# Kernel tuning notes

Hardware: AMD Instinct MI355X
Metric: run time of the kernel (lower is better)

The kernel has to match this reference:

```python
import jax, jax.numpy as jnp
import numpy as np

N, D, H, DH, E = 50000, 128, 4, 32, 600000
EPS = 1e-5


def _seg_softmax(logits, seg, n):
    # numerically stable softmax over edges grouped by destination node
    m = jax.ops.segment_max(logits, seg, num_segments=n)
    e = jnp.exp(logits - m[seg])
    s = jax.ops.segment_sum(e, seg, num_segments=n)
    return e / s[seg]


def _bn(x, g, b):
    # BatchNorm1d, training-mode statistics (biased variance), eps=1e-5
    mu = jnp.mean(x, 0)
    var = jnp.mean((x - mu) ** 2, 0)
    return g * (x - mu) * jax.lax.rsqrt(var + EPS) + b


def _gat(x, src, dst, W, a_s, a_d, bias):
    # PyG GATConv: shared lin, additive attention, leaky_relu(0.2), dst-softmax, concat heads + bias
    n = x.shape[0]
    xp = (x @ W).reshape(n, H, DH)
    al_s = jnp.sum(xp * a_s, -1)  # [N,H]
    al_d = jnp.sum(xp * a_d, -1)
    lg = jax.nn.leaky_relu(al_s[src] + al_d[dst], 0.2)  # [E',H]
    alpha = _seg_softmax(lg, dst, n)
    out = jax.ops.segment_sum(alpha[..., None] * xp[src], dst, num_segments=n)
    return out.reshape(n, H * DH) + bias


def setup_inputs() -> dict:
    key = jax.random.key(0)
    ks = jax.random.split(key, 24)
    s = 0.05
    inp = {
        'x_cell': jax.random.normal(ks[0], (N, D), jnp.float32),
        'z_h': jax.random.normal(ks[1], (D,), jnp.float32),
        'x_cell_embedded': jax.random.normal(ks[2], (N, D), jnp.float32),
        'edge_index_0': jax.random.randint(ks[3], (2, E), 0, N, dtype=jnp.int32),
        'edge_index_1': jax.random.randint(ks[4], (2, E), 0, N, dtype=jnp.int32),
        # GAT params, stacked over (conv layer 0/1, edge type 0/1)
        'gat_W': jax.random.normal(ks[5], (2, 2, D, D), jnp.float32) * s,
        'gat_att_src': jax.random.normal(ks[6], (2, 2, H, DH), jnp.float32) * s,
        'gat_att_dst': jax.random.normal(ks[7], (2, 2, H, DH), jnp.float32) * s,
        'gat_bias': jnp.zeros((2, 2, D), jnp.float32),
        # BatchNorm params for bn1, bn2, bn_hgt
        'bn_gamma': jnp.ones((3, D), jnp.float32),
        'bn_beta': jnp.zeros((3, D), jnp.float32),
        # HGTConv params
        'hgt_Wk': jax.random.normal(ks[8], (D, D), jnp.float32) * s,
        'hgt_bk': jnp.zeros((D,), jnp.float32),
        'hgt_Wq': jax.random.normal(ks[9], (D, D), jnp.float32) * s,
        'hgt_bq': jnp.zeros((D,), jnp.float32),
        'hgt_Wv': jax.random.normal(ks[10], (D, D), jnp.float32) * s,
        'hgt_bv': jnp.zeros((D,), jnp.float32),
        'hgt_a_rel': jax.random.normal(ks[11], (2, H, DH, DH), jnp.float32) * s,
        'hgt_m_rel': jax.random.normal(ks[12], (2, H, DH, DH), jnp.float32) * s,
        'hgt_p_rel': jnp.ones((2, H), jnp.float32),
        'hgt_Wo': jax.random.normal(ks[13], (D, D), jnp.float32) * s,
        'hgt_bo': jnp.zeros((D,), jnp.float32),
        'hgt_skip': jnp.float32(1.0),
        # input injection + FiLM
        'inj_W': jax.random.normal(ks[14], (D, D), jnp.float32) * s,
        'inj_b': jnp.zeros((D,), jnp.float32),
        'film_W1': jax.random.normal(ks[15], (D, 2 * D), jnp.float32) * s,
        'film_b1': jnp.zeros((2 * D,), jnp.float32),
        'film_W2': jax.random.normal(ks[16], (2 * D, 2 * D), jnp.float32) * s,
        'film_b2': jnp.zeros((2 * D,), jnp.float32),
    }
    return inp


def reference(x_cell, z_h, x_cell_embedded, edge_index_0, edge_index_1,
              gat_W, gat_att_src, gat_att_dst, gat_bias, bn_gamma, bn_beta,
              hgt_Wk, hgt_bk, hgt_Wq, hgt_bq, hgt_Wv, hgt_bv,
              hgt_a_rel, hgt_m_rel, hgt_p_rel, hgt_Wo, hgt_bo, hgt_skip,
              inj_W, inj_b, film_W1, film_b1, film_W2, film_b2):
    n = x_cell.shape[0]
    loops = jnp.arange(n, dtype=edge_index_0.dtype)
    # GATConv add_self_loops=True: augment each relation's edge list with self loops
    eis = [(jnp.concatenate([ei[0], loops]), jnp.concatenate([ei[1], loops]))
           for ei in (edge_index_0, edge_index_1)]

    def hetero_gat(x, c):
        out = jnp.zeros((n, D), x.dtype)
        for t, (src, dst) in enumerate(eis):  # HeteroConv aggr='sum'
            out = out + _gat(x, src, dst, gat_W[c, t], gat_att_src[c, t], gat_att_dst[c, t], gat_bias[c, t])
        return out

    lrelu = lambda v: jax.nn.leaky_relu(v, 0.2)
    x1 = lrelu(x_cell + _bn(hetero_gat(x_cell, 0), bn_gamma[0], bn_beta[0]))
    x2 = lrelu(x1 + _bn(hetero_gat(x1, 1), bn_gamma[1], bn_beta[1]))

    # HGTConv (single node type, 2 edge types, no self loops)
    k = (x2 @ hgt_Wk + hgt_bk).reshape(n, H, DH)
    q = (x2 @ hgt_Wq + hgt_bq).reshape(n, H, DH)
    v = (x2 @ hgt_Wv + hgt_bv).reshape(n, H, DH)
    lgs, msgs, dsts = [], [], []
    inv_sqrt = np.float32(1.0 / np.sqrt(DH))
    for t, ei in enumerate((edge_index_0, edge_index_1)):
        src, dst = ei[0], ei[1]
        kt = jnp.einsum('nhd,hde->nhe', k, hgt_a_rel[t])  # relation-transformed keys
        vt = jnp.einsum('nhd,hde->nhe', v, hgt_m_rel[t])  # relation-transformed values
        lgs.append(jnp.sum(q[dst] * kt[src], -1) * hgt_p_rel[t] * inv_sqrt)  # [E,H]
        msgs.append(vt[src])
        dsts.append(dst)
    lg = jnp.concatenate(lgs)
    msg = jnp.concatenate(msgs)
    dst_all = jnp.concatenate(dsts)
    alpha = _seg_softmax(lg, dst_all, n)  # softmax over all incoming edges (all relations)
    agg = jax.ops.segment_sum(alpha[..., None] * msg, dst_all, num_segments=n).reshape(n, H * DH)
    hgt_out = jax.nn.gelu(agg, approximate=False) @ hgt_Wo + hgt_bo
    sk = jax.nn.sigmoid(hgt_skip)
    x3 = sk * hgt_out + (1.0 - sk) * x2

    x3 = _bn(x3, bn_gamma[2], bn_beta[2])
    x3 = lrelu(x2 + x3)
    x3 = x3 + x_cell_embedded @ inj_W + inj_b

    # FiLM on global z_h
    hzh = jax.nn.gelu(z_h @ film_W1 + film_b1, approximate=False)
    gb = hzh @ film_W2 + film_b2
    gamma, beta = gb[:D], gb[D:]
    return gamma * x3 + beta
```

## Files before the change

kernel.cpp:

```cpp
#include <hip/hip_runtime.h>
#include <math.h>

#define NN 50000
#define DD 128
#define HH 4
#define DHH 32
#define EE 600000
#define N2 (2*NN)
#define NBLK 256

typedef unsigned short u16;
typedef unsigned int   u32;
using short8 = __attribute__((ext_vector_type(8))) short;
using f32x4  = __attribute__((ext_vector_type(4))) float;

#define LOG2E 1.44269504f

__device__ __forceinline__ float lrelu(float v){ return v > 0.f ? v : 0.2f*v; }
__device__ __forceinline__ float gelu_exact(float x){ return 0.5f*x*(1.f+erff(x*0.70710678118654752f)); }
__device__ __forceinline__ u16 f2bf(float f){
  u32 u = __float_as_uint(f);
  u32 r = (u + 0x7fffu + ((u>>16)&1u)) >> 16;
  return (u16)r;
}
__device__ __forceinline__ u32 pack2bf(float a, float b){ return (u32)f2bf(a) | ((u32)f2bf(b)<<16); }
__device__ __forceinline__ float bflo(u32 u){ return __uint_as_float(u<<16); }
__device__ __forceinline__ float bfhi(u32 u){ return __uint_as_float(u & 0xffff0000u); }

__global__ __launch_bounds__(256) void prep_all(
    const float* __restrict__ gat_W, const float* __restrict__ Wk, const float* __restrict__ Wv,
    const float* __restrict__ Wo, const float* __restrict__ injW, u16* __restrict__ WT,
    const float* __restrict__ Wq, const float* __restrict__ bq, const float* __restrict__ a_rel,
    u16* __restrict__ wqtT, float* __restrict__ bqt,
    const float* __restrict__ z, const float* __restrict__ fW1, const float* __restrict__ fb1,
    const float* __restrict__ fW2, const float* __restrict__ fb2, float* __restrict__ gb){
  __shared__ float t[32][33];
  __shared__ float hsh[256];
  const int bid = blockIdx.x;
  if(bid < 128){
    const int m = bid >> 4, tile = bid & 15, tr = tile>>2, tc = tile&3;
    const float* src = (m<4) ? (gat_W + (size_t)m*16384) : (m==4? Wk : m==5? Wv : m==6? Wo : injW);
    const int lr = threadIdx.x>>5, lc = threadIdx.x&31;
    #pragma unroll
    for(int p=0;p<4;++p) t[lr+p*8][lc] = src[(size_t)(tr*32+lr+p*8)*128 + tc*32+lc];
    __syncthreads();
    #pragma unroll
    for(int p=0;p<4;++p)
      WT[(size_t)m*16384 + (size_t)(tc*32+lr+p*8)*128 + tr*32+lc] = f2bf(t[lc][lr+p*8]);
  } else if(bid < 257){
    int idx = (bid-128)*256 + threadIdx.x;
    if(idx < 2*128*129){
      int tt = idx / (128*129);
      int r = idx % (128*129);
      int f = r / 129, c = r % 129;
      int h = f>>5, m = f&31;
      const float* srcp = (c<128) ? (Wq + (size_t)c*128 + h*DHH) : (bq + h*DHH);
      const float* arow = a_rel + (((size_t)(tt*HH+h)*DHH)+m)*DHH;
      float s=0.f;
      #pragma unroll
      for(int e=0;e<DHH;++e) s = fmaf(srcp[e], arow[e], s);
      if(c<128) wqtT[(size_t)tt*16384 + (size_t)f*128 + c] = f2bf(s);
      else      bqt[tt*128 + f] = s;
    }
  } else {
    int j = threadIdx.x;
    float acc = fb1[j];
    for(int d=0; d<DD; ++d) acc = fmaf(z[d], fW1[d*256+j], acc);
    hsh[j] = gelu_exact(acc);
    __syncthreads();
    float acc2 = fb2[j];
    for(int k=0;k<256;++k) acc2 = fmaf(hsh[k], fW2[k*256+j], acc2);
    gb[j] = acc2;
  }
}

__global__ void count2_kernel(const int* __restrict__ d0, const int* __restrict__ d1, int* __restrict__ jcnt){
  int e = blockIdx.x*blockDim.x+threadIdx.x;
  if(e < EE)        atomicAdd(&jcnt[d0[e]], 1);
  else if(e < 2*EE) atomicAdd(&jcnt[NN + d1[e-EE]], 1);
}

__global__ void scan_partial(const int* __restrict__ cnt, int* __restrict__ bsum){
  int t = threadIdx.x;
  int i0 = blockIdx.x*512 + 2*t;
  int s = 0;
  if(i0   < N2) s += cnt[i0];
  if(i0+1 < N2) s += cnt[i0+1];
  __shared__ int red[256];
  red[t]=s; __syncthreads();
  for(int off=128; off>0; off>>=1){ if(t<off) red[t]+=red[t+off]; __syncthreads(); }
  if(t==0) bsum[blockIdx.x]=red[0];
}

__global__ void scan_final2(const int* __restrict__ cnt, const int* __restrict__ bsum,
                            int* __restrict__ jrs, int* __restrict__ jcur, int nb){
  __shared__ int sh[256];
  int t = threadIdx.x;
  {
    int v = (t<nb)? bsum[t] : 0;
    sh[t]=v; __syncthreads();
    for(int off=1; off<256; off<<=1){
      int u = (t>=off)? sh[t-off] : 0; __syncthreads();
      sh[t]+=u; __syncthreads();
    }
  }
  const int bofsv = sh[blockIdx.x] - bsum[blockIdx.x];
  if(blockIdx.x==0 && t==0) jrs[N2] = sh[nb-1];
  __syncthreads();
  int i0 = blockIdx.x*512 + 2*t;
  int a = (i0   < N2)? cnt[i0]   : 0;
  int c = (i0+1 < N2)? cnt[i0+1] : 0;
  int s = a+c;
  sh[t]=s; __syncthreads();
  for(int off=1; off<256; off<<=1){
    int u = (t>=off)? sh[t-off] : 0; __syncthreads();
    sh[t]+=u; __syncthreads();
  }
  int ex = bofsv + sh[t]-s;
  if(i0   < N2){ jrs[i0]=ex;     jcur[i0]=ex; }
  if(i0+1 < N2){ jrs[i0+1]=ex+a; jcur[i0+1]=ex+a; }
}

__global__ void fill2_kernel(const int* __restrict__ ei0, const int* __restrict__ ei1,
                             int* __restrict__ jcur, u16* __restrict__ es){
  int e = blockIdx.x*blockDim.x+threadIdx.x;
  if(e < EE){
    int d = ei0[EE+e];
    int pos = atomicAdd(&jcur[d],1);
    es[pos] = (u16)ei0[e];
  } else if(e < 2*EE){
    int i = e-EE;
    int d = ei1[EE+i];
    int pos = atomicAdd(&jcur[NN+d],1);
    es[pos] = (u16)ei1[i];
  }
}

constexpr int MM_BIAS  = 1;
constexpr int MM_FILM  = 2;
constexpr int MM_SKIP  = 4;
constexpr int MM_ATT   = 8;
constexpr int MM_ABF16 = 64;

#define SWZ(row, byte) ((byte) ^ (((row)&7)<<4))

template<int MODE>
__device__ __forceinline__ void mgemm_core(const void* Av, const u16* WT, int row0, int n,
                                           u16* Al, u16* Wl, f32x4 (&acc)[8]){
  const int tid = threadIdx.x;
  if(MODE & MM_ABF16){
    const uint2* Ag = (const uint2*)((const u16*)Av + (size_t)row0*128);
    const int maxv = (min(64, n-row0))*32;
    #pragma unroll
    for(int j=0;j<8;++j){
      int v = tid + j*256;
      uint2 st = make_uint2(0u,0u);
      if(v < maxv) st = Ag[v];
      int row = v>>5, cb = (v&31)*8;
      *(uint2*)((char*)Al + row*256 + SWZ(row, cb)) = st;
    }
  } else {
    const float4* Ag = (const float4*)((const float*)Av + (size_t)row0*128);
    const int maxv = (min(64, n-row0))*32;
    #pragma unroll
    for(int j=0;j<8;++j){
      int v = tid + j*256;
      float4 val = make_float4(0.f,0.f,0.f,0.f);
      if(v < maxv) val = Ag[v];
      int row = v>>5, cb = (v&31)*8;
      uint2 st; st.x = pack2bf(val.x, val.y); st.y = pack2bf(val.z, val.w);
      *(uint2*)((char*)Al + row*256 + SWZ(row, cb)) = st;
    }
  }
  {
    const u32* Wg = (const u32*)WT;
    #pragma unroll
    for(int j=0;j<32;++j){
      int v = tid + j*256;
      u32 w = Wg[v];
      int row = v>>6, cb = (v&63)*4;
      *(u32*)((char*)Wl + row*256 + SWZ(row, cb)) = w;
    }
  }
  __syncthreads();
  const int lane = tid & 63;
  const int wv   = tid >> 6;
  const int r16  = lane & 15;
  const int kg   = lane >> 4;
  #pragma unroll
  for(int nn=0;nn<8;++nn) acc[nn] = (f32x4){0.f,0.f,0.f,0.f};
  #pragma unroll
  for(int s=0;s<4;++s){
    const int arow = wv*16 + r16;
    const int kb = s*64 + kg*16;
    short8 af = *(const short8*)((const char*)Al + arow*256 + SWZ(arow, kb));
    #pragma unroll
    for(int nn=0;nn<8;++nn){
      const int brow = nn*16 + r16;
      short8 bf = *(const short8*)((const char*)Wl + brow*256 + SWZ(brow, kb));
      acc[nn] = __builtin_amdgcn_mfma_f32_16x16x32_bf16(af, bf, acc[nn], 0, 0, 0);
    }
  }
}

template<int MODE>
__global__ __launch_bounds__(256) void mgemm(const void* __restrict__ Av, const u16* __restrict__ WT,
    const float* __restrict__ bias, const float* __restrict__ base, const float* __restrict__ fgb,
    const float* __restrict__ skipv, float* __restrict__ C, int n){
  __shared__ u16 Al[64*128];
  __shared__ u16 Wl[128*128];
  const int row0 = blockIdx.x*64;
  f32x4 acc[8];
  mgemm_core<MODE>(Av, WT, row0, n, Al, Wl, acc);
  const int lane = threadIdx.x & 63;
  const int wv   = threadIdx.x >> 6;
  const int r16  = lane & 15;
  const int kg   = lane >> 4;
  float bvals[8];
  if(MODE & MM_BIAS){
    #pragma unroll
    for(int nn=0;nn<8;++nn) bvals[nn] = bias[nn*16+r16];
  }
  float sk = 0.f;
  if(MODE & MM_SKIP) sk = 1.f/(1.f+__expf(-skipv[0]));
  #pragma unroll
  for(int i=0;i<4;++i){
    const int row = row0 + wv*16 + kg*4 + i;
    if(row >= n) continue;
    #pragma unroll
    for(int nn=0;nn<8;++nn){
      const int col = nn*16 + r16;
      float o = acc[nn][i];
      if(MODE & MM_BIAS) o += bvals[nn];
      if(MODE & MM_SKIP)
        o = sk*o + (1.f-sk)*base[(size_t)row*128 + col];
      if(MODE & MM_FILM){
        o += base[(size_t)row*128 + col];
        o = fgb[col]*o + fgb[128+col];
      }
      C[(size_t)row*128 + col] = o;
    }
  }
}

struct MJob {
  const u16* WT;
  const float* bias;
  const float* as_;
  const float* ad_;
  void* Cv;
  int att_t;
  int sel;
};
struct MJobs { MJob j[4]; };

template<int MODE>
__global__ __launch_bounds__(256) void mgemmJ(const float* __restrict__ Av, MJobs jobs,
    float* __restrict__ als8, float* __restrict__ ald8, int blocksPerJob, int n){
  __shared__ u16 Al[64*128];
  __shared__ u16 Wl[128*128];
  const MJob job = jobs.j[blockIdx.x / blocksPerJob];
  const int row0 = (blockIdx.x % blocksPerJob)*64;
  f32x4 acc[8];
  mgemm_core<MODE>(Av, job.WT, row0, n, Al, Wl, acc);
  const int lane = threadIdx.x & 63;
  const int wv   = threadIdx.x >> 6;
  const int r16  = lane & 15;
  const int kg   = lane >> 4;
  if(MODE & MM_ATT){
    float asv[8], adv[8];
    #pragma unroll
    for(int nn=0;nn<8;++nn){ asv[nn]=job.as_[nn*16+r16]; adv[nn]=job.ad_[nn*16+r16]; }
    #pragma unroll
    for(int i=0;i<4;++i){
      const int row = row0 + wv*16 + kg*4 + i;
      #pragma unroll
      for(int h=0;h<4;++h){
        float ps = asv[2*h]*acc[2*h][i] + asv[2*h+1]*acc[2*h+1][i];
        float pd = adv[2*h]*acc[2*h][i] + adv[2*h+1]*acc[2*h+1][i];
        ps += __shfl_xor(ps,1); ps += __shfl_xor(ps,2); ps += __shfl_xor(ps,4); ps += __shfl_xor(ps,8);
        pd += __shfl_xor(pd,1); pd += __shfl_xor(pd,2); pd += __shfl_xor(pd,4); pd += __shfl_xor(pd,8);
        if(row < n && r16 == 0){
          als8[(size_t)row*8 + 2*h + job.att_t] = ps;
          ald8[(size_t)row*8 + 2*h + job.att_t] = pd;
        }
      }
    }
  }
  float bvals[8];
  if(MODE & MM_BIAS){
    #pragma unroll
    for(int nn=0;nn<8;++nn) bvals[nn] = job.bias[nn*16+r16];
  }
  #pragma unroll
  for(int i=0;i<4;++i){
    const int row = row0 + wv*16 + kg*4 + i;
    if(row >= n) continue;
    #pragma unroll
    for(int nn=0;nn<8;++nn){
      const int col = nn*16 + r16;
      float o = acc[nn][i];
      if(MODE & MM_BIAS) o += bvals[nn];
      if(job.sel == 1)
        ((u16*)job.Cv)[(size_t)row*128 + col] = f2bf(o);
      else
        *(u16*)((char*)job.Cv + (size_t)row*512 + (col>>1)*8 + (col&1)*2 + (job.sel-2)*4) = f2bf(o);
    }
  }
}

__global__ __launch_bounds__(256) void gat_gather3(const u16* __restrict__ xp0, const u16* __restrict__ xp1,
    const float* __restrict__ als8, const float* __restrict__ ald8,
    const int* __restrict__ jrs, const u16* __restrict__ es,
    const float* __restrict__ gb0, const float* __restrict__ gb1, float* __restrict__ out){
  const int gid = blockIdx.x*blockDim.x + threadIdx.x;
  const int node = gid >> 6;
  const int lane = threadIdx.x & 63;
  if(node >= NN) return;
  const int h = lane >> 4;
  const int cc = 2*lane;
  float o0 = gb0[cc] + gb1[cc], o1 = gb0[cc+1] + gb1[cc+1];
  #pragma unroll
  for(int t=0;t<2;++t){
    const u16* __restrict__ xp = t ? xp1 : xp0;
    const float aldv = ald8[(size_t)node*8 + 2*h + t];
    const int s0 = jrs[t*NN+node], s1 = jrs[t*NN+node+1];
    float ssum=0.f, a0=0.f, a1=0.f;
    int p = s0;
    for(; p+3<s1; p+=4){
      const int sA = es[p], sB = es[p+1], sC = es[p+2], sD = es[p+3];
      const u32 xA = *(const u32*)&xp[(size_t)sA*DD + cc];
      const u32 xB = *(const u32*)&xp[(size_t)sB*DD + cc];
      const u32 xC = *(const u32*)&xp[(size_t)sC*DD + cc];
      const u32 xD = *(const u32*)&xp[(size_t)sD*DD + cc];
      float lA = als8[(size_t)sA*8 + 2*h + t] + aldv;
      float lB = als8[(size_t)sB*8 + 2*h + t] + aldv;
      float lC = als8[(size_t)sC*8 + 2*h + t] + aldv;
      float lD = als8[(size_t)sD*8 + 2*h + t] + aldv;
      const float eA = exp2f(lA>0.f ? lA*LOG2E : lA*(0.2f*LOG2E));
      const float eB = exp2f(lB>0.f ? lB*LOG2E : lB*(0.2f*LOG2E));
      const float eC = exp2f(lC>0.f ? lC*LOG2E : lC*(0.2f*LOG2E));
      const float eD = exp2f(lD>0.f ? lD*LOG2E : lD*(0.2f*LOG2E));
      ssum += (eA+eB)+(eC+eD);
      a0 = fmaf(eA, bflo(xA), a0); a1 = fmaf(eA, bfhi(xA), a1);
      a0 = fmaf(eB, bflo(xB), a0); a1 = fmaf(eB, bfhi(xB), a1);
      a0 = fmaf(eC, bflo(xC), a0); a1 = fmaf(eC, bfhi(xC), a1);
      a0 = fmaf(eD, bflo(xD), a0); a1 = fmaf(eD, bfhi(xD), a1);
    }
    for(; p<s1; ++p){
      const int sA = es[p];
      const u32 xA = *(const u32*)&xp[(size_t)sA*DD + cc];
      float lA = als8[(size_t)sA*8 + 2*h + t] + aldv;
      const float eA = exp2f(lA>0.f ? lA*LOG2E : lA*(0.2f*LOG2E));
      ssum += eA;
      a0 = fmaf(eA, bflo(xA), a0); a1 = fmaf(eA, bfhi(xA), a1);
    }
    {
      float lg = als8[(size_t)node*8 + 2*h + t] + aldv;
      const float ev = exp2f(lg>0.f ? lg*LOG2E : lg*(0.2f*LOG2E));
      ssum += ev;
      const u32 xr = *(const u32*)&xp[(size_t)node*DD + cc];
      a0 = fmaf(ev, bflo(xr), a0); a1 = fmaf(ev, bfhi(xr), a1);
    }
    const float inv = 1.f/ssum;
    o0 = fmaf(a0, inv, o0); o1 = fmaf(a1, inv, o1);
  }
  *(float2*)&out[(size_t)node*DD + cc] = make_float2(o0, o1);
}

__global__ __launch_bounds__(256) void bn_stats_fused(const float* __restrict__ X, float* __restrict__ part,
                               const float* __restrict__ gamma, const float* __restrict__ beta,
                               float* __restrict__ stat, int* __restrict__ counter){
  const int f = threadIdx.x & 127, rg = threadIdx.x>>7;
  float s=0.f, s2=0.f;
  for(int r = blockIdx.x*2+rg; r<NN; r += NBLK*2){
    float v = X[(size_t)r*DD+f]; s+=v; s2 = fmaf(v,v,s2);
  }
  __shared__ float ls[256], ls2[256];
  __shared__ int lastsh;
  ls[threadIdx.x]=s; ls2[threadIdx.x]=s2; __syncthreads();
  if(rg==0){
    part[blockIdx.x*256 + f]       = ls[f]+ls[128+f];
    part[blockIdx.x*256 + 128 + f] = ls2[f]+ls2[128+f];
  }
  __threadfence();
  if(threadIdx.x==0) lastsh = (atomicAdd(counter,1) == NBLK-1);
  __syncthreads();
  if(lastsh){
    __threadfence();
    float ss=0.f, ss2=0.f;
    #pragma unroll 8
    for(int bk=rg; bk<NBLK; bk+=2){
      ss  += part[bk*256 + f];
      ss2 += part[bk*256 + 128 + f];
    }
    __syncthreads();
    ls[threadIdx.x]=ss; ls2[threadIdx.x]=ss2;
    __syncthreads();
    if(rg==0){
      float S1 = ls[f]+ls[128+f], S2 = ls2[f]+ls2[128+f];
      float mu = S1/(float)NN;
      float var = S2/(float)NN - mu*mu;
      float rs = rsqrtf(var+1e-5f);
      stat[f]     = gamma[f]*rs;
      stat[128+f] = beta[f] - gamma[f]*rs*mu;
    }
    if(threadIdx.x==0) *counter = 0;
  }
}

__global__ void bn_apply_lrelu(const float* __restrict__ xprev, const float* __restrict__ acc,
                               const float* __restrict__ stat, float* __restrict__ out){
  int idx = blockIdx.x*blockDim.x+threadIdx.x;
  if(idx >= NN*64) return;
  int c = (2*idx) & 127;
  float2 x = ((const float2*)xprev)[idx];
  float2 a = ((const float2*)acc)[idx];
  float o0 = lrelu(x.x + fmaf(stat[c],   a.x, stat[128+c]));
  float o1 = lrelu(x.y + fmaf(stat[c+1], a.y, stat[128+c+1]));
  ((float2*)out)[idx] = make_float2(o0,o1);
}

__global__ __launch_bounds__(256) void hgt_merged2(const u16* __restrict__ qt,
    const u32* __restrict__ kv, const int* __restrict__ jrs, const u16* __restrict__ es,
    const float* __restrict__ p_rel, u16* __restrict__ Sv){
  const int gid = blockIdx.x*blockDim.x + threadIdx.x;
  const int node = gid >> 6;
  const int lane = threadIdx.x & 63;
  if(node >= NN) return;
  const int h = lane >> 4;
  float acc[2][2] = {{0.f,0.f},{0.f,0.f}};
  float ssum = 0.f;
  #pragma unroll
  for(int t=0;t<2;++t){
    const u32 qw = *(const u32*)&qt[(size_t)t*NN*DD + (size_t)node*DD + 2*lane];
    const float q0 = bflo(qw), q1 = bfhi(qw);
    const float scale2 = p_rel[t*HH+h]*(0.17677669529663687f*LOG2E);
    const int s0 = jrs[t*NN+node], s1 = jrs[t*NN+node+1];
    int p = s0;
    for(; p+3<s1; p+=4){
      const int sA = es[p], sB = es[p+1], sC = es[p+2], sD = es[p+3];
      const uint2 kA = *(const uint2*)&kv[(size_t)sA*128 + 2*lane];
      const uint2 kB = *(const uint2*)&kv[(size_t)sB*128 + 2*lane];
      const uint2 kC = *(const uint2*)&kv[(size_t)sC*128 + 2*lane];
      const uint2 kD = *(const uint2*)&kv[(size_t)sD*128 + 2*lane];
      float pA = q0*bflo(kA.x) + q1*bfhi(kA.x);
      float pB = q0*bflo(kB.x) + q1*bfhi(kB.x);
      float pC = q0*bflo(kC.x) + q1*bfhi(kC.x);
      float pD = q0*bflo(kD.x) + q1*bfhi(kD.x);
      pA += __shfl_xor(pA,1); pB += __shfl_xor(pB,1); pC += __shfl_xor(pC,1); pD += __shfl_xor(pD,1);
      pA += __shfl_xor(pA,2); pB += __shfl_xor(pB,2); pC += __shfl_xor(pC,2); pD += __shfl_xor(pD,2);
      pA += __shfl_xor(pA,4); pB += __shfl_xor(pB,4); pC += __shfl_xor(pC,4); pD += __shfl_xor(pD,4);
      pA += __shfl_xor(pA,8); pB += __shfl_xor(pB,8); pC += __shfl_xor(pC,8); pD += __shfl_xor(pD,8);
      const float eA=exp2f(pA*scale2), eB=exp2f(pB*scale2);
      const float eC=exp2f(pC*scale2), eD=exp2f(pD*scale2);
      ssum += (eA+eB)+(eC+eD);
      acc[t][0] = fmaf(eA, bflo(kA.y), acc[t][0]); acc[t][1] = fmaf(eA, bfhi(kA.y), acc[t][1]);
      acc[t][0] = fmaf(eB, bflo(kB.y), acc[t][0]); acc[t][1] = fmaf(eB, bfhi(kB.y), acc[t][1]);
      acc[t][0] = fmaf(eC, bflo(kC.y), acc[t][0]); acc[t][1] = fmaf(eC, bfhi(kC.y), acc[t][1]);
      acc[t][0] = fmaf(eD, bflo(kD.y), acc[t][0]); acc[t][1] = fmaf(eD, bfhi(kD.y), acc[t][1]);
    }
    for(; p<s1; ++p){
      const int sA = es[p];
      const uint2 kA = *(const uint2*)&kv[(size_t)sA*128 + 2*lane];
      float pA = q0*bflo(kA.x) + q1*bfhi(kA.x);
      pA += __shfl_xor(pA,1); pA += __shfl_xor(pA,2); pA += __shfl_xor(pA,4); pA += __shfl_xor(pA,8);
      const float eA = exp2f(pA*scale2);
      ssum += eA;
      acc[t][0] = fmaf(eA, bflo(kA.y), acc[t][0]); acc[t][1] = fmaf(eA, bfhi(kA.y), acc[t][1]);
    }
  }
  const float inv = ssum>0.f ? 1.f/ssum : 0.f;
  ((u32*)&Sv[(size_t)node*256 +       2*lane])[0] = pack2bf(acc[0][0]*inv, acc[0][1]*inv);
  ((u32*)&Sv[(size_t)node*256 + 128 + 2*lane])[0] = pack2bf(acc[1][0]*inv, acc[1][1]*inv);
}

__global__ __launch_bounds__(256) void mtransform_kernel(const u16* __restrict__ Sv, const float* __restrict__ m_rel,
                                                         u16* __restrict__ out){
  __shared__ float Msh[2*HH*DHH*DHH];
  for(int i=threadIdx.x;i<2*HH*DHH*DHH;i+=256) Msh[i]=m_rel[i];
  __syncthreads();
  int idx = blockIdx.x*blockDim.x + threadIdx.x;
  if(idx >= NN*DD) return;
  int node = idx>>7, f = idx&127, h = f>>5, e = f&31;
  const u16* s0p = &Sv[(size_t)node*256 + h*DHH];
  const u16* s1p = &Sv[(size_t)node*256 + 128 + h*DHH];
  const float* M0 = &Msh[(0*HH+h)*DHH*DHH + e];
  const float* M1 = &Msh[(1*HH+h)*DHH*DHH + e];
  float s = 0.f;
  #pragma unroll
  for(int d=0; d<DHH; d+=2){
    u32 w0 = *(const u32*)&s0p[d];
    u32 w1 = *(const u32*)&s1p[d];
    s = fmaf(bflo(w0), M0[d*DHH],     s);
    s = fmaf(bfhi(w0), M0[(d+1)*DHH], s);
    s = fmaf(bflo(w1), M1[d*DHH],     s);
    s = fmaf(bfhi(w1), M1[(d+1)*DHH], s);
  }
  out[idx] = f2bf(gelu_exact(s));
}

extern "C" void kernel_launch(void* const* d_in, const int* in_sizes, int n_in,
                              void* d_out, int out_size, void* d_ws, size_t ws_size,
                              hipStream_t stream){
  const float* x_cell = (const float*)d_in[0];
  const float* z_h    = (const float*)d_in[1];
  const float* x_emb  = (const float*)d_in[2];
  const int*   ei0    = (const int*)d_in[3];
  const int*   ei1    = (const int*)d_in[4];
  const float* gat_W  = (const float*)d_in[5];
  const float* gat_as = (const float*)d_in[6];
  const float* gat_ad = (const float*)d_in[7];
  const float* gat_b  = (const float*)d_in[8];
  const float* bn_g   = (const float*)d_in[9];
  const float* bn_b   = (const float*)d_in[10];
  const float* Wk = (const float*)d_in[11];
  const float* bk = (const float*)d_in[12];
  const float* Wq = (const float*)d_in[13];
  const float* bq = (const float*)d_in[14];
  const float* Wv = (const float*)d_in[15];
  const float* bv = (const float*)d_in[16];
  const float* a_rel = (const float*)d_in[17];
  const float* m_rel = (const float*)d_in[18];
  const float* p_rel = (const float*)d_in[19];
  const float* Wo = (const float*)d_in[20];
  const float* bo = (const float*)d_in[21];
  const float* skip = (const float*)d_in[22];
  const float* injW = (const float*)d_in[23];
  const float* injb = (const float*)d_in[24];
  const float* fW1 = (const float*)d_in[25];
  const float* fb1 = (const float*)d_in[26];
  const float* fW2 = (const float*)d_in[27];
  const float* fb2 = (const float*)d_in[28];

  constexpr size_t SLOT = (size_t)NN*DD;
  float* ws = (float*)d_ws;
  float* A    = ws;
  float* X2   = A + SLOT;
  float* als8 = X2 + SLOT;
  float* ald8 = als8 + (size_t)NN*8;
  float* bnpart = ald8 + (size_t)NN*8;
  float* bnstat = bnpart + 256*256;
  float* fgb    = bnstat + 256;
  float* bqt    = fgb + 256;
  u16* WT8  = (u16*)(bqt + 2*128);
  u16* WQT  = WT8 + (size_t)8*16384;
  u16* S    = WQT + (size_t)2*16384;
  u16* XP0  = S + (size_t)NN*256;
  u16* XP1  = XP0 + SLOT;
  u16* es   = XP1 + SLOT;
  int* jcnt = (int*)(es + (size_t)2*EE + 2);
  int* bnctr= jcnt + N2;
  int* jrs  = bnctr + 4;
  int* jcur = jrs + N2 + 2;
  int* bsum = jcur + N2;
  size_t needed = (size_t)((char*)(bsum + 256) - (char*)d_ws);
  if(ws_size < needed) return;

  u16* QT = (u16*)A;
  u16* MT = (u16*)A;
  u32* KV = (u32*)XP0;

  const int TB = 256;
  dim3 b(TB);
  const int gE2    = (2*EE + TB - 1)/TB;
  const int gND    = (NN*DD + TB - 1)/TB;
  const int gND2   = (NN*64 + TB - 1)/TB;
  const int gNodes = (NN + 3)/4;
  const int gMG    = (NN + 63)/64;
  const int gScan  = (N2 + 511)/512;

  prep_all<<<258, b, 0, stream>>>(gat_W, Wk, Wv, Wo, injW, WT8, Wq, bq, a_rel, WQT, bqt,
                                  z_h, fW1, fb1, fW2, fb2, fgb);

  hipMemsetAsync(jcnt, 0, (N2+4)*sizeof(int), stream);
  count2_kernel<<<gE2, b, 0, stream>>>(ei0+EE, ei1+EE, jcnt);
  scan_partial<<<gScan, b, 0, stream>>>(jcnt, bsum);
  scan_final2<<<gScan, b, 0, stream>>>(jcnt, bsum, jrs, jcur, gScan);
  fill2_kernel<<<gE2, b, 0, stream>>>(ei0, ei1, jcur, es);

  const float* xin = x_cell;
  for(int c=0;c<2;++c){
    MJobs gj{};
    for(int t=0;t<2;++t){
      gj.j[t].WT   = WT8 + (size_t)(c*2+t)*16384;
      gj.j[t].bias = nullptr;
      gj.j[t].as_  = gat_as + (size_t)(c*2+t)*HH*DHH;
      gj.j[t].ad_  = gat_ad + (size_t)(c*2+t)*HH*DHH;
      gj.j[t].Cv   = t? (void*)XP1 : (void*)XP0;
      gj.j[t].att_t = t;
      gj.j[t].sel  = 1;
    }
    mgemmJ<MM_ATT><<<2*gMG, b, 0, stream>>>(xin, gj, als8, ald8, gMG, NN);
    gat_gather3<<<gNodes, b, 0, stream>>>(XP0, XP1, als8, ald8, jrs, es,
        gat_b + (size_t)(c*2+0)*DD, gat_b + (size_t)(c*2+1)*DD, A);
    bn_stats_fused<<<NBLK, b, 0, stream>>>(A, bnpart, bn_g + (size_t)c*DD, bn_b + (size_t)c*DD, bnstat, bnctr);
    bn_apply_lrelu<<<gND2, b, 0, stream>>>(xin, A, bnstat, X2);
    xin = X2;
  }
  float* x2 = X2;

  {
    MJobs hj{};
    hj.j[0] = { WQT,             bqt,       nullptr, nullptr, (void*)QT,          0, 1 };
    hj.j[1] = { WQT + 16384,     bqt + 128, nullptr, nullptr, (void*)(QT + SLOT), 0, 1 };
    hj.j[2] = { WT8 + (size_t)4*16384, bk,  nullptr, nullptr, (void*)KV,          0, 2 };
    hj.j[3] = { WT8 + (size_t)5*16384, bv,  nullptr, nullptr, (void*)KV,          0, 3 };
    mgemmJ<MM_BIAS><<<4*gMG, b, 0, stream>>>(x2, hj, nullptr, nullptr, gMG, NN);
  }
  hgt_merged2<<<gNodes, b, 0, stream>>>(QT, KV, jrs, es, p_rel, S);
  mtransform_kernel<<<gND, b, 0, stream>>>(S, m_rel, MT);
  mgemm<MM_ABF16|MM_BIAS|MM_SKIP><<<gMG, b, 0, stream>>>(MT, WT8 + (size_t)6*16384, bo,
      x2, nullptr, skip, (float*)d_out, NN);
  bn_stats_fused<<<NBLK, b, 0, stream>>>((float*)d_out, bnpart, bn_g + 2*DD, bn_b + 2*DD, bnstat, bnctr);
  bn_apply_lrelu<<<gND2, b, 0, stream>>>(x2, (float*)d_out, bnstat, (float*)d_out);
  mgemm<MM_BIAS|MM_FILM><<<gMG, b, 0, stream>>>(x_emb, WT8 + (size_t)7*16384, injb,
      (float*)d_out, fgb, nullptr, (float*)d_out, NN);
}
```

Measured before the change: 781.8 us.

## Share A-tile across GEMM jobs per block and store HGT K/V in fp8

Result: faster. 760.6 us (-2.7%).

```diff
diff --git a/kernel.cpp b/kernel.cpp
--- a/kernel.cpp
+++ b/kernel.cpp
@@ -11,8 +11,10 @@
 
 typedef unsigned short u16;
 typedef unsigned int   u32;
+typedef unsigned char  u8;
 using short8 = __attribute__((ext_vector_type(8))) short;
 using f32x4  = __attribute__((ext_vector_type(4))) float;
+using f32x2  = __attribute__((ext_vector_type(2))) float;
 
 #define LOG2E 1.44269504f
 
@@ -139,7 +141,6 @@
 constexpr int MM_BIAS  = 1;
 constexpr int MM_FILM  = 2;
 constexpr int MM_SKIP  = 4;
-constexpr int MM_ATT   = 8;
 constexpr int MM_ABF16 = 64;
 
 #define SWZ(row, byte) ((byte) ^ (((row)&7)<<4))
@@ -254,58 +255,97 @@
 };
 struct MJobs { MJob j[4]; };
 
-template<int MODE>
-__global__ __launch_bounds__(256) void mgemmJ(const float* __restrict__ Av, MJobs jobs,
-    float* __restrict__ als8, float* __restrict__ ald8, int blocksPerJob, int n){
+__global__ __launch_bounds__(256) void mgemmM(const float* __restrict__ Av, MJobs jobs, int njobs,
+    float* __restrict__ als8, float* __restrict__ ald8, int n){
   __shared__ u16 Al[64*128];
   __shared__ u16 Wl[128*128];
-  const MJob job = jobs.j[blockIdx.x / blocksPerJob];
-  const int row0 = (blockIdx.x % blocksPerJob)*64;
-  f32x4 acc[8];
-  mgemm_core<MODE>(Av, job.WT, row0, n, Al, Wl, acc);
-  const int lane = threadIdx.x & 63;
-  const int wv   = threadIdx.x >> 6;
+  const int tid = threadIdx.x;
+  const int row0 = blockIdx.x*64;
+  {
+    const float4* Ag = (const float4*)(Av + (size_t)row0*128);
+    const int maxv = (min(64, n-row0))*32;
+    #pragma unroll
+    for(int j=0;j<8;++j){
+      int v = tid + j*256;
+      float4 val = make_float4(0.f,0.f,0.f,0.f);
+      if(v < maxv) val = Ag[v];
+      int row = v>>5, cb = (v&31)*8;
+      uint2 st; st.x = pack2bf(val.x, val.y); st.y = pack2bf(val.z, val.w);
+      *(uint2*)((char*)Al + row*256 + SWZ(row, cb)) = st;
+    }
+  }
+  const int lane = tid & 63;
+  const int wv   = tid >> 6;
   const int r16  = lane & 15;
   const int kg   = lane >> 4;
-  if(MODE & MM_ATT){
-    float asv[8], adv[8];
-    #pragma unroll
-    for(int nn=0;nn<8;++nn){ asv[nn]=job.as_[nn*16+r16]; adv[nn]=job.ad_[nn*16+r16]; }
+  for(int jj=0; jj<njobs; ++jj){
+    const MJob job = jobs.j[jj];
+    {
+      const u32* Wg = (const u32*)job.WT;
+      #pragma unroll
+      for(int j=0;j<32;++j){
+        int v = tid + j*256;
+        u32 w = Wg[v];
+        int row = v>>6, cb = (v&63)*4;
+        *(u32*)((char*)Wl + row*256 + SWZ(row, cb)) = w;
+      }
+    }
+    __syncthreads();
+    f32x4 acc[8];
+    #pragma unroll
+    for(int nn=0;nn<8;++nn) acc[nn] = (f32x4){0.f,0.f,0.f,0.f};
+    #pragma unroll
+    for(int s=0;s<4;++s){
+      const int arow = wv*16 + r16;
+      const int kb = s*64 + kg*16;
+      short8 af = *(const short8*)((const char*)Al + arow*256 + SWZ(arow, kb));
+      #pragma unroll
+      for(int nn=0;nn<8;++nn){
+        const int brow = nn*16 + r16;
+        short8 bf = *(const short8*)((const char*)Wl + brow*256 + SWZ(brow, kb));
+        acc[nn] = __builtin_amdgcn_mfma_f32_16x16x32_bf16(af, bf, acc[nn], 0, 0, 0);
+      }
+    }
+    if(job.as_){
+      float asv[8], adv[8];
+      #pragma unroll
+      for(int nn=0;nn<8;++nn){ asv[nn]=job.as_[nn*16+r16]; adv[nn]=job.ad_[nn*16+r16]; }
+      #pragma unroll
+      for(int i=0;i<4;++i){
+        const int row = row0 + wv*16 + kg*4 + i;
+        #pragma unroll
+        for(int h=0;h<4;++h){
+          float ps = asv[2*h]*acc[2*h][i] + asv[2*h+1]*acc[2*h+1][i];
+          float pd = adv[2*h]*acc[2*h][i] + adv[2*h+1]*acc[2*h+1][i];
+          ps += __shfl_xor(ps,1); ps += __shfl_xor(ps,2); ps += __shfl_xor(ps,4); ps += __shfl_xor(ps,8);
+          pd += __shfl_xor(pd,1); pd += __shfl_xor(pd,2); pd += __shfl_xor(pd,4); pd += __shfl_xor(pd,8);
+          if(row < n && r16 == 0){
+            als8[(size_t)row*8 + 2*h + job.att_t] = ps;
+            ald8[(size_t)row*8 + 2*h + job.att_t] = pd;
+          }
+        }
+      }
+    }
+    float bvals[8];
+    #pragma unroll
+    for(int nn=0;nn<8;++nn) bvals[nn] = job.bias ? job.bias[nn*16+r16] : 0.f;
     #pragma unroll
     for(int i=0;i<4;++i){
       const int row = row0 + wv*16 + kg*4 + i;
+      if(row >= n) continue;
       #pragma unroll
-      for(int h=0;h<4;++h){
-        float ps = asv[2*h]*acc[2*h][i] + asv[2*h+1]*acc[2*h+1][i];
-        float pd = adv[2*h]*acc[2*h][i] + adv[2*h+1]*acc[2*h+1][i];
-        ps += __shfl_xor(ps,1); ps += __shfl_xor(ps,2); ps += __shfl_xor(ps,4); ps += __shfl_xor(ps,8);
-        pd += __shfl_xor(pd,1); pd += __shfl_xor(pd,2); pd += __shfl_xor(pd,4); pd += __shfl_xor(pd,8);
-        if(row < n && r16 == 0){
-          als8[(size_t)row*8 + 2*h + job.att_t] = ps;
-          ald8[(size_t)row*8 + 2*h + job.att_t] = pd;
+      for(int nn=0;nn<8;++nn){
+        const int col = nn*16 + r16;
+        float o = acc[nn][i] + bvals[nn];
+        if(job.sel == 1){
+          ((u16*)job.Cv)[(size_t)row*128 + col] = f2bf(o);
+        } else {
+          u32 enc = __builtin_amdgcn_cvt_pk_fp8_f32(o, 0.f, 0u, false);
+          ((u8*)job.Cv)[(size_t)row*256 + (col>>1)*4 + (col&1) + (job.sel-2)*2] = (u8)(enc & 0xffu);
         }
       }
     }
-  }
-  float bvals[8];
-  if(MODE & MM_BIAS){
-    #pragma unroll
-    for(int nn=0;nn<8;++nn) bvals[nn] = job.bias[nn*16+r16];
-  }
-  #pragma unroll
-  for(int i=0;i<4;++i){
-    const int row = row0 + wv*16 + kg*4 + i;
-    if(row >= n) continue;
-    #pragma unroll
-    for(int nn=0;nn<8;++nn){
-      const int col = nn*16 + r16;
-      float o = acc[nn][i];
-      if(MODE & MM_BIAS) o += bvals[nn];
-      if(job.sel == 1)
-        ((u16*)job.Cv)[(size_t)row*128 + col] = f2bf(o);
-      else
-        *(u16*)((char*)job.Cv + (size_t)row*512 + (col>>1)*8 + (col&1)*2 + (job.sel-2)*4) = f2bf(o);
-    }
+    __syncthreads();
   }
 }
 
@@ -440,14 +480,22 @@
     int p = s0;
     for(; p+3<s1; p+=4){
       const int sA = es[p], sB = es[p+1], sC = es[p+2], sD = es[p+3];
-      const uint2 kA = *(const uint2*)&kv[(size_t)sA*128 + 2*lane];
-      const uint2 kB = *(const uint2*)&kv[(size_t)sB*128 + 2*lane];
-      const uint2 kC = *(const uint2*)&kv[(size_t)sC*128 + 2*lane];
-      const uint2 kD = *(const uint2*)&kv[(size_t)sD*128 + 2*lane];
-      float pA = q0*bflo(kA.x) + q1*bfhi(kA.x);
-      float pB = q0*bflo(kB.x) + q1*bfhi(kB.x);
-      float pC = q0*bflo(kC.x) + q1*bfhi(kC.x);
-      float pD = q0*bflo(kD.x) + q1*bfhi(kD.x);
+      const u32 wA = kv[(size_t)sA*64 + lane];
+      const u32 wB = kv[(size_t)sB*64 + lane];
+      const u32 wC = kv[(size_t)sC*64 + lane];
+      const u32 wD = kv[(size_t)sD*64 + lane];
+      f32x2 kA = __builtin_amdgcn_cvt_pk_f32_fp8(wA, false);
+      f32x2 kB = __builtin_amdgcn_cvt_pk_f32_fp8(wB, false);
+      f32x2 kC = __builtin_amdgcn_cvt_pk_f32_fp8(wC, false);
+      f32x2 kD = __builtin_amdgcn_cvt_pk_f32_fp8(wD, false);
+      f32x2 vA = __builtin_amdgcn_cvt_pk_f32_fp8(wA, true);
+      f32x2 vB = __builtin_amdgcn_cvt_pk_f32_fp8(wB, true);
+      f32x2 vC = __builtin_amdgcn_cvt_pk_f32_fp8(wC, true);
+      f32x2 vD = __builtin_amdgcn_cvt_pk_f32_fp8(wD, true);
+      float pA = q0*kA.x + q1*kA.y;
+      float pB = q0*kB.x + q1*kB.y;
+      float pC = q0*kC.x + q1*kC.y;
+      float pD = q0*kD.x + q1*kD.y;
       pA += __shfl_xor(pA,1); pB += __shfl_xor(pB,1); pC += __shfl_xor(pC,1); pD += __shfl_xor(pD,1);
       pA += __shfl_xor(pA,2); pB += __shfl_xor(pB,2); pC += __shfl_xor(pC,2); pD += __shfl_xor(pD,2);
       pA += __shfl_xor(pA,4); pB += __shfl_xor(pB,4); pC += __shfl_xor(pC,4); pD += __shfl_xor(pD,4);
@@ -455,19 +503,21 @@
       const float eA=exp2f(pA*scale2), eB=exp2f(pB*scale2);
       const float eC=exp2f(pC*scale2), eD=exp2f(pD*scale2);
       ssum += (eA+eB)+(eC+eD);
-      acc[t][0] = fmaf(eA, bflo(kA.y), acc[t][0]); acc[t][1] = fmaf(eA, bfhi(kA.y), acc[t][1]);
-      acc[t][0] = fmaf(eB, bflo(kB.y), acc[t][0]); acc[t][1] = fmaf(eB, bfhi(kB.y), acc[t][1]);
-      acc[t][0] = fmaf(eC, bflo(kC.y), acc[t][0]); acc[t][1] = fmaf(eC, bfhi(kC.y), acc[t][1]);
-      acc[t][0] = fmaf(eD, bflo(kD.y), acc[t][0]); acc[t][1] = fmaf(eD, bfhi(kD.y), acc[t][1]);
+      acc[t][0] = fmaf(eA, vA.x, acc[t][0]); acc[t][1] = fmaf(eA, vA.y, acc[t][1]);
+      acc[t][0] = fmaf(eB, vB.x, acc[t][0]); acc[t][1] = fmaf(eB, vB.y, acc[t][1]);
+      acc[t][0] = fmaf(eC, vC.x, acc[t][0]); acc[t][1] = fmaf(eC, vC.y, acc[t][1]);
+      acc[t][0] = fmaf(eD, vD.x, acc[t][0]); acc[t][1] = fmaf(eD, vD.y, acc[t][1]);
     }
     for(; p<s1; ++p){
       const int sA = es[p];
-      const uint2 kA = *(const uint2*)&kv[(size_t)sA*128 + 2*lane];
-      float pA = q0*bflo(kA.x) + q1*bfhi(kA.x);
+      const u32 wA = kv[(size_t)sA*64 + lane];
+      f32x2 kA = __builtin_amdgcn_cvt_pk_f32_fp8(wA, false);
+      f32x2 vA = __builtin_amdgcn_cvt_pk_f32_fp8(wA, true);
+      float pA = q0*kA.x + q1*kA.y;
       pA += __shfl_xor(pA,1); pA += __shfl_xor(pA,2); pA += __shfl_xor(pA,4); pA += __shfl_xor(pA,8);
       const float eA = exp2f(pA*scale2);
       ssum += eA;
-      acc[t][0] = fmaf(eA, bflo(kA.y), acc[t][0]); acc[t][1] = fmaf(eA, bfhi(kA.y), acc[t][1]);
+      acc[t][0] = fmaf(eA, vA.x, acc[t][0]); acc[t][1] = fmaf(eA, vA.y, acc[t][1]);
     }
   }
   const float inv = ssum>0.f ? 1.f/ssum : 0.f;
@@ -591,7 +641,7 @@
       gj.j[t].att_t = t;
       gj.j[t].sel  = 1;
     }
-    mgemmJ<MM_ATT><<<2*gMG, b, 0, stream>>>(xin, gj, als8, ald8, gMG, NN);
+    mgemmM<<<gMG, b, 0, stream>>>(xin, gj, 2, als8, ald8, NN);
     gat_gather3<<<gNodes, b, 0, stream>>>(XP0, XP1, als8, ald8, jrs, es,
         gat_b + (size_t)(c*2+0)*DD, gat_b + (size_t)(c*2+1)*DD, A);
     bn_stats_fused<<<NBLK, b, 0, stream>>>(A, bnpart, bn_g + (size_t)c*DD, bn_b + (size_t)c*DD, bnstat, bnctr);
@@ -602,11 +652,11 @@
 
   {
     MJobs hj{};
-    hj.j[0] = { WQT,             bqt,       nullptr, nullptr, (void*)QT,          0, 1 };
-    hj.j[1] = { WQT + 16384,     bqt + 128, nullptr, nullptr, (void*)(QT + SLOT), 0, 1 };
-    hj.j[2] = { WT8 + (size_t)4*16384, bk,  nullptr, nullptr, (void*)KV,          0, 2 };
-    hj.j[3] = { WT8 + (size_t)5*16384, bv,  nullptr, nullptr, (void*)KV,          0, 3 };
-    mgemmJ<MM_BIAS><<<4*gMG, b, 0, stream>>>(x2, hj, nullptr, nullptr, gMG, NN);
+    hj.j[0] = { WQT,                   bqt,       nullptr, nullptr, (void*)QT,          0, 1 };
+    hj.j[1] = { WQT + 16384,           bqt + 128, nullptr, nullptr, (void*)(QT + SLOT), 0, 1 };
+    hj.j[2] = { WT8 + (size_t)4*16384, bk,        nullptr, nullptr, (void*)KV,          0, 2 };
+    hj.j[3] = { WT8 + (size_t)5*16384, bv,        nullptr, nullptr, (void*)KV,          0, 3 };
+    mgemmM<<<gMG, b, 0, stream>>>(x2, hj, 4, nullptr, nullptr, NN);
   }
   hgt_merged2<<<gNodes, b, 0, stream>>>(QT, KV, jrs, es, p_rel, S);
   mtransform_kernel<<<gND, b, 0, stream>>>(S, m_rel, MT);
```
